# Performance work log

Hardware: AMD Instinct MI355X
Metric: run time of the kernel (lower is better)

## Reference

```python
import jax, jax.numpy as jnp
import numpy as np

EPS = 1e-6  # nn.PairwiseDistance default eps, added as x - y + eps before the norm


def setup_inputs() -> dict:
    key = jax.random.key(0)
    k1, k2 = jax.random.split(key)
    class_prototypes = jax.random.normal(k1, (1024, 1024), dtype=jnp.float32)
    query_features = jax.random.normal(k2, (8192, 1024), dtype=jnp.float32)
    return {"class_prototypes": class_prototypes, "query_features": query_features}


def reference(class_prototypes, query_features):
    # dist[i,k] = || q_i - p_k + EPS ||_2  (PairwiseDistance semantics)
    # expand: ||q||^2 + ||p||^2 - 2 q.p + 2*EPS*(sum q - sum p) + D*EPS^2
    D = query_features.shape[1]
    q_sq = jnp.sum(query_features * query_features, axis=1)        # [Q]
    p_sq = jnp.sum(class_prototypes * class_prototypes, axis=1)    # [K]
    cross = query_features @ class_prototypes.T                    # [Q,K]
    lin = 2.0 * EPS * (jnp.sum(query_features, axis=1)[:, None]
                       - jnp.sum(class_prototypes, axis=1)[None, :])
    sq = q_sq[:, None] + p_sq[None, :] - 2.0 * cross + lin + D * EPS * EPS
    dist = jnp.sqrt(jnp.maximum(sq, 0.0))                          # [Q,K]
    post = jnp.exp(-dist)
    post = post / jnp.sum(post, axis=1, keepdims=True)
    c = jnp.max(post, axis=1)
    h = -jnp.sum(post * jnp.log(post), axis=1)
    return (post, c, h)
```

## Files before the change

kernel.cpp:

```cpp
#include <hip/hip_runtime.h>
#include <hip/hip_bf16.h>

#define EPS 1e-6f

typedef float  f32x4  __attribute__((ext_vector_type(4)));
typedef __bf16 bf16x8 __attribute__((ext_vector_type(8)));

static __device__ __forceinline__ unsigned short f2bf(float f) {
    unsigned int x = __float_as_uint(f);
    unsigned int r = (x + 0x7FFFu + ((x >> 16) & 1u)) >> 16;
    return (unsigned short)r;
}
static __device__ __forceinline__ float bf2f(unsigned short u) {
    return __uint_as_float((unsigned int)u << 16);
}

__global__ __launch_bounds__(256) void prep_kernel(
    const float* __restrict__ protos, const float* __restrict__ querys,
    unsigned short* __restrict__ pb, unsigned short* __restrict__ qb,
    float* __restrict__ p_sq, float* __restrict__ p_sum,
    float* __restrict__ q_sq, float* __restrict__ q_sum)
{
    const int b   = blockIdx.x;
    const int tid = threadIdx.x;
    const float* src; unsigned short* dst; float* rsq; float* rsum;
    if (b < 1024) {
        src = protos + (size_t)b * 1024; dst = pb + (size_t)b * 1024;
        rsq = p_sq + b; rsum = p_sum + b;
    } else {
        const int r = b - 1024;
        src = querys + (size_t)r * 1024; dst = qb + (size_t)r * 1024;
        rsq = q_sq + r; rsum = q_sum + r;
    }

    const float4 v = reinterpret_cast<const float4*>(src)[tid];
    float s  = v.x + v.y + v.z + v.w;
    float ss = v.x * v.x + v.y * v.y + v.z * v.z + v.w * v.w;

    ushort4 o;
    o.x = f2bf(v.x); o.y = f2bf(v.y); o.z = f2bf(v.z); o.w = f2bf(v.w);
    reinterpret_cast<ushort4*>(dst)[tid] = o;

    #pragma unroll
    for (int m = 32; m >= 1; m >>= 1) {
        s  += __shfl_xor(s, m, 64);
        ss += __shfl_xor(ss, m, 64);
    }
    __shared__ float red[8];
    const int wave = tid >> 6;
    if ((tid & 63) == 0) { red[wave] = s; red[4 + wave] = ss; }
    __syncthreads();
    if (tid == 0) {
        *rsum = red[0] + red[1] + red[2] + red[3];
        *rsq  = red[4] + red[5] + red[6] + red[7];
    }
}

__global__ __launch_bounds__(256, 2) void gemm_exp_kernel(
    const unsigned short* __restrict__ qb,
    const unsigned short* __restrict__ pb,
    const float* __restrict__ q_sq, const float* __restrict__ q_sum,
    const float* __restrict__ p_sq, const float* __restrict__ p_sum,
    unsigned short* __restrict__ e_out,
    float* __restrict__ row_s, float* __restrict__ row_t,
    unsigned int* __restrict__ row_m)
{
    __shared__ unsigned short As[128 * 64];
    __shared__ unsigned short Bs[128 * 64];

    const int tid  = threadIdx.x;
    const int lane = tid & 63;
    const int wave = tid >> 6;
    const int wr = wave >> 1, wc = wave & 1;
    const int l15 = lane & 15;
    const int l4  = lane >> 4;

    const int hwid  = blockIdx.x + blockIdx.y * 64;
    const int newid = (hwid & 7) * 64 + (hwid >> 3);
    const int bx = newid >> 3;
    const int by = newid & 7;

    f32x4 acc[4][4];
    #pragma unroll
    for (int m = 0; m < 4; ++m)
        #pragma unroll
        for (int n = 0; n < 4; ++n)
            acc[m][n] = (f32x4)0.0f;

    const size_t qbase = (size_t)(bx * 128) * 1024;
    const size_t pbase = (size_t)(by * 128) * 1024;

    for (int kk = 0; kk < 1024; kk += 64) {
        __syncthreads();
        #pragma unroll
        for (int i = 0; i < 4; ++i) {
            const int lin = i * 256 + tid;
            const int row = lin >> 3;
            const int cg  = (lin & 7) ^ (row & 7);
            const unsigned short* ga = qb + qbase + (size_t)row * 1024 + kk + cg * 8;
            const unsigned short* gb = pb + pbase + (size_t)row * 1024 + kk + cg * 8;
            __builtin_amdgcn_global_load_lds((const __attribute__((address_space(1))) void*)ga,
                                             (__attribute__((address_space(3))) void*)(&As[lin * 8]), 16, 0, 0);
            __builtin_amdgcn_global_load_lds((const __attribute__((address_space(1))) void*)gb,
                                             (__attribute__((address_space(3))) void*)(&Bs[lin * 8]), 16, 0, 0);
        }
        __syncthreads();

        #pragma unroll
        for (int s = 0; s < 2; ++s) {
            bf16x8 a[4], b[4];
            #pragma unroll
            for (int m = 0; m < 4; ++m) {
                const int rowA = wr * 64 + m * 16 + l15;
                const int ca = (s * 4 + l4) ^ (rowA & 7);
                a[m] = *reinterpret_cast<const bf16x8*>(&As[rowA * 64 + ca * 8]);
            }
            #pragma unroll
            for (int n = 0; n < 4; ++n) {
                const int rowB = wc * 64 + n * 16 + l15;
                const int cb = (s * 4 + l4) ^ (rowB & 7);
                b[n] = *reinterpret_cast<const bf16x8*>(&Bs[rowB * 64 + cb * 8]);
            }
            #pragma unroll
            for (int m = 0; m < 4; ++m)
                #pragma unroll
                for (int n = 0; n < 4; ++n)
                    acc[m][n] = __builtin_amdgcn_mfma_f32_16x16x32_bf16(a[m], b[n], acc[m][n], 0, 0, 0);
        }
    }

    const int row0 = bx * 128 + wr * 64;
    const int col0 = by * 128 + wc * 64;

    float ps[4], pm[4];
    #pragma unroll
    for (int n = 0; n < 4; ++n) {
        const int c = col0 + n * 16 + l15;
        ps[n] = p_sq[c];
        pm[n] = p_sum[c];
    }
    const float dee = 1024.0f * EPS * EPS;

    #pragma unroll
    for (int m = 0; m < 4; ++m) {
        #pragma unroll
        for (int r = 0; r < 4; ++r) {
            const int row = row0 + m * 16 + l4 * 4 + r;
            const float qs = q_sq[row], qm = q_sum[row];
            float se = 0.0f, te = 0.0f, mx = 0.0f;
            #pragma unroll
            for (int n = 0; n < 4; ++n) {
                const float cross = acc[m][n][r];
                const float sq = qs + ps[n] - 2.0f * cross + 2.0f * EPS * (qm - pm[n]) + dee;
                const float dist = sqrtf(fmaxf(sq, 0.0f));
                const float e = __expf(-dist);
                e_out[(size_t)row * 1024 + (col0 + n * 16 + l15)] = f2bf(e);
                se += e;
                te += e * dist;
                mx = fmaxf(mx, e);
            }
            #pragma unroll
            for (int msk = 8; msk >= 1; msk >>= 1) {
                se += __shfl_xor(se, msk, 64);
                te += __shfl_xor(te, msk, 64);
                mx = fmaxf(mx, __shfl_xor(mx, msk, 64));
            }
            if (l15 == 0) {
                atomicAdd(&row_s[row], se);
                atomicAdd(&row_t[row], te);
                atomicMax(&row_m[row], __float_as_uint(mx));
            }
        }
    }
}

__global__ __launch_bounds__(256) void normfin_kernel(
    const unsigned short* __restrict__ e16,
    const float* __restrict__ row_s, const float* __restrict__ row_t,
    const unsigned int* __restrict__ row_m,
    float* __restrict__ post, float* __restrict__ c_out, float* __restrict__ h_out)
{
    const int row = blockIdx.x;
    const int tid = threadIdx.x;
    const float s   = row_s[row];
    const float inv = 1.0f / s;
    if (tid == 0) {
        c_out[row] = __uint_as_float(row_m[row]) * inv;
        h_out[row] = logf(s) + row_t[row] * inv;
    }
    const ushort4 ev = reinterpret_cast<const ushort4*>(e16 + (size_t)row * 1024)[tid];
    float4 o;
    o.x = bf2f(ev.x) * inv;
    o.y = bf2f(ev.y) * inv;
    o.z = bf2f(ev.z) * inv;
    o.w = bf2f(ev.w) * inv;
    reinterpret_cast<float4*>(post + (size_t)row * 1024)[tid] = o;
}

extern "C" void kernel_launch(void* const* d_in, const int* in_sizes, int n_in,
                              void* d_out, int out_size, void* d_ws, size_t ws_size,
                              hipStream_t stream) {
    const float* protos = (const float*)d_in[0];
    const float* querys = (const float*)d_in[1];

    float* out   = (float*)d_out;
    float* post  = out;
    float* c_out = out + (size_t)8192 * 1024;
    float* h_out = c_out + 8192;

    char* ws = (char*)d_ws;
    unsigned short* qb  = (unsigned short*)ws;  ws += (size_t)8192 * 1024 * 2;
    unsigned short* pb  = (unsigned short*)ws;  ws += (size_t)1024 * 1024 * 2;
    unsigned short* e16 = (unsigned short*)ws;  ws += (size_t)8192 * 1024 * 2;
    float* q_sq  = (float*)ws;  ws += 8192 * 4;
    float* q_sum = (float*)ws;  ws += 8192 * 4;
    float* p_sq  = (float*)ws;  ws += 1024 * 4;
    float* p_sum = (float*)ws;  ws += 1024 * 4;
    float* row_s = (float*)ws;  ws += 8192 * 4;
    float* row_t = (float*)ws;  ws += 8192 * 4;
    unsigned int* row_m = (unsigned int*)ws;  ws += 8192 * 4;

    (void)hipMemsetAsync(row_s, 0, 3 * 8192 * sizeof(float), stream);

    prep_kernel<<<9216, 256, 0, stream>>>(protos, querys, pb, qb, p_sq, p_sum, q_sq, q_sum);
    gemm_exp_kernel<<<dim3(64, 8), 256, 0, stream>>>(qb, pb, q_sq, q_sum, p_sq, p_sum,
                                                     e16, row_s, row_t, row_m);
    normfin_kernel<<<8192, 256, 0, stream>>>(e16, row_s, row_t, row_m, post, c_out, h_out);
}
```

Before: 129.7 us.

## Pipeline GEMM K-loop with 4-stage LDS ring buffer and async prefetch

Replaces the synchronous load-then-compute K loop (64-wide tiles, two barriers per step) with a 4-buffer ring of 32-wide K tiles. Loads are issued two stages ahead and guarded by s_waitcnt vmcnt plus a single barrier per step, so global-to-LDS transfers overlap MFMA work. The swizzle changes to suit the 32-wide rows. LDS use stays at 32KB, but correctness now depends on the manual vmcnt accounting and on the ring depth being enough to avoid overwriting a buffer another wave is still reading.

```diff
diff --git a/kernel.cpp b/kernel.cpp
--- a/kernel.cpp
+++ b/kernel.cpp
@@ -65,8 +65,8 @@
     float* __restrict__ row_s, float* __restrict__ row_t,
     unsigned int* __restrict__ row_m)
 {
-    __shared__ unsigned short As[128 * 64];
-    __shared__ unsigned short Bs[128 * 64];
+    __shared__ unsigned short As[4][128 * 32];
+    __shared__ unsigned short Bs[4][128 * 32];
 
     const int tid  = threadIdx.x;
     const int lane = tid & 63;
@@ -90,44 +90,67 @@
     const size_t qbase = (size_t)(bx * 128) * 1024;
     const size_t pbase = (size_t)(by * 128) * 1024;
 
-    for (int kk = 0; kk < 1024; kk += 64) {
-        __syncthreads();
-        #pragma unroll
-        for (int i = 0; i < 4; ++i) {
-            const int lin = i * 256 + tid;
-            const int row = lin >> 3;
-            const int cg  = (lin & 7) ^ (row & 7);
-            const unsigned short* ga = qb + qbase + (size_t)row * 1024 + kk + cg * 8;
-            const unsigned short* gb = pb + pbase + (size_t)row * 1024 + kk + cg * 8;
-            __builtin_amdgcn_global_load_lds((const __attribute__((address_space(1))) void*)ga,
-                                             (__attribute__((address_space(3))) void*)(&As[lin * 8]), 16, 0, 0);
-            __builtin_amdgcn_global_load_lds((const __attribute__((address_space(1))) void*)gb,
-                                             (__attribute__((address_space(3))) void*)(&Bs[lin * 8]), 16, 0, 0);
-        }
-        __syncthreads();
-
-        #pragma unroll
-        for (int s = 0; s < 2; ++s) {
-            bf16x8 a[4], b[4];
-            #pragma unroll
-            for (int m = 0; m < 4; ++m) {
-                const int rowA = wr * 64 + m * 16 + l15;
-                const int ca = (s * 4 + l4) ^ (rowA & 7);
-                a[m] = *reinterpret_cast<const bf16x8*>(&As[rowA * 64 + ca * 8]);
-            }
-            #pragma unroll
-            for (int n = 0; n < 4; ++n) {
-                const int rowB = wc * 64 + n * 16 + l15;
-                const int cb = (s * 4 + l4) ^ (rowB & 7);
-                b[n] = *reinterpret_cast<const bf16x8*>(&Bs[rowB * 64 + cb * 8]);
-            }
-            #pragma unroll
-            for (int m = 0; m < 4; ++m)
-                #pragma unroll
-                for (int n = 0; n < 4; ++n)
-                    acc[m][n] = __builtin_amdgcn_mfma_f32_16x16x32_bf16(a[m], b[n], acc[m][n], 0, 0, 0);
-        }
-    }
+#define STAGE(BUF, KK) do {                                                              \
+    const int la0 = tid, la1 = tid + 256;                                                \
+    const int kp0 = (la0 & 3) ^ ((la0 >> 3) & 3);                                        \
+    const int kp1 = (la1 & 3) ^ ((la1 >> 3) & 3);                                        \
+    const unsigned short* ga0 = qb + qbase + (size_t)(la0 >> 2) * 1024 + (KK) + kp0 * 8; \
+    const unsigned short* ga1 = qb + qbase + (size_t)(la1 >> 2) * 1024 + (KK) + kp1 * 8; \
+    const unsigned short* gb0 = pb + pbase + (size_t)(la0 >> 2) * 1024 + (KK) + kp0 * 8; \
+    const unsigned short* gb1 = pb + pbase + (size_t)(la1 >> 2) * 1024 + (KK) + kp1 * 8; \
+    __builtin_amdgcn_global_load_lds((const __attribute__((address_space(1))) void*)ga0, \
+        (__attribute__((address_space(3))) void*)(&As[BUF][la0 * 8]), 16, 0, 0);         \
+    __builtin_amdgcn_global_load_lds((const __attribute__((address_space(1))) void*)ga1, \
+        (__attribute__((address_space(3))) void*)(&As[BUF][la1 * 8]), 16, 0, 0);         \
+    __builtin_amdgcn_global_load_lds((const __attribute__((address_space(1))) void*)gb0, \
+        (__attribute__((address_space(3))) void*)(&Bs[BUF][la0 * 8]), 16, 0, 0);         \
+    __builtin_amdgcn_global_load_lds((const __attribute__((address_space(1))) void*)gb1, \
+        (__attribute__((address_space(3))) void*)(&Bs[BUF][la1 * 8]), 16, 0, 0);         \
+} while (0)
+
+#define COMPUTE(BUF) do {                                                                \
+    bf16x8 a[4], b[4];                                                                   \
+    _Pragma("unroll")                                                                    \
+    for (int m = 0; m < 4; ++m) {                                                        \
+        const int rowA = wr * 64 + m * 16 + l15;                                         \
+        a[m] = *reinterpret_cast<const bf16x8*>(                                         \
+            &As[BUF][rowA * 32 + (l4 ^ ((rowA >> 1) & 3)) * 8]);                         \
+    }                                                                                    \
+    _Pragma("unroll")                                                                    \
+    for (int n = 0; n < 4; ++n) {                                                        \
+        const int rowB = wc * 64 + n * 16 + l15;                                         \
+        b[n] = *reinterpret_cast<const bf16x8*>(                                         \
+            &Bs[BUF][rowB * 32 + (l4 ^ ((rowB >> 1) & 3)) * 8]);                         \
+    }                                                                                    \
+    _Pragma("unroll")                                                                    \
+    for (int m = 0; m < 4; ++m)                                                          \
+        _Pragma("unroll")                                                                \
+        for (int n = 0; n < 4; ++n)                                                      \
+            acc[m][n] = __builtin_amdgcn_mfma_f32_16x16x32_bf16(a[m], b[n], acc[m][n], 0, 0, 0); \
+} while (0)
+
+    STAGE(0, 0);
+    STAGE(1, 32);
+
+    #pragma unroll 1
+    for (int i = 0; i < 30; ++i) {
+        STAGE((i + 2) & 3, (i + 2) * 32);
+        asm volatile("s_waitcnt vmcnt(8)" ::: "memory");
+        __builtin_amdgcn_s_barrier();
+        __builtin_amdgcn_sched_barrier(0);
+        COMPUTE(i & 3);
+    }
+    asm volatile("s_waitcnt vmcnt(4)" ::: "memory");
+    __builtin_amdgcn_s_barrier();
+    __builtin_amdgcn_sched_barrier(0);
+    COMPUTE(2);
+    asm volatile("s_waitcnt vmcnt(0)" ::: "memory");
+    __builtin_amdgcn_s_barrier();
+    __builtin_amdgcn_sched_barrier(0);
+    COMPUTE(3);
+
+#undef STAGE
+#undef COMPUTE
 
     const int row0 = bx * 128 + wr * 64;
     const int col0 = by * 128 + wc * 64;
```

Result: slower. 133.6 us (+3.0%).
